# Performance work log

Hardware: AMD Instinct MI355X
Metric: run time of the kernel (lower is better)

## Reference

```python
import jax, jax.numpy as jnp
import numpy as np

M, N, B, L = 512, 2048, 4, 20
H_DENSITY = 0.02  # Tanner graph sparsity: row weight ~N*p=40, col weight ~M*p=10


def setup_inputs() -> dict:
    key = jax.random.key(0)
    ks = jax.random.split(key, 10)
    H = jax.random.bernoulli(ks[0], H_DENSITY, (M, N)).astype(jnp.float32)
    llrs = jax.random.uniform(ks[1], (N,), jnp.float32)
    syndromes = jax.random.randint(ks[2], (B, M, 1), 0, 2, jnp.int32)
    errors = jax.random.randint(ks[3], (B, N), 0, 2, jnp.int32)
    weights_de = jax.random.uniform(ks[4], (L, M, N), jnp.float32)
    weights_llr = jax.random.uniform(ks[5], (L, N), jnp.float32)
    marg_weights_de = jax.random.uniform(ks[6], (L, M, N), jnp.float32)
    marg_weights_llr = jax.random.uniform(ks[7], (L, N), jnp.float32)
    rhos = jnp.ones((L,), jnp.float32)
    residual_weights = jnp.zeros((L,), jnp.float32)
    return dict(syndromes=syndromes, errors=errors, H=H, llrs=llrs,
                weights_de=weights_de, weights_llr=weights_llr,
                marg_weights_de=marg_weights_de, marg_weights_llr=marg_weights_llr,
                rhos=rhos, residual_weights=residual_weights)


def reference(syndromes, errors, H, llrs, weights_de, weights_llr,
              marg_weights_de, marg_weights_llr, rhos, residual_weights):
    batch = syndromes.shape[0]
    m, n = H.shape
    rhos_norm = jax.nn.softmax(rhos)                       # (L,)
    sign = 1.0 - 2.0 * syndromes.astype(H.dtype)           # (B,m,1): (-1)**syndrome
    err_f = errors.astype(H.dtype)                         # (B,n)
    eps = 1e-6

    def step(msgs_dn, xs):
        w_de, w_llr, mw_de, mw_llr, rho, rw = xs
        # error-node (variable) update: column-sum minus self, masked by H
        msgs_en = (H * (llrs * w_llr)
                   + jnp.sum(msgs_dn * w_de, axis=1, keepdims=True)) * H - msgs_dn
        # detector-node (check) update: tanh-product rule with self-exclusion
        d = jnp.tanh(msgs_en * 0.5)
        d = jnp.where(d == 0, jnp.asarray(1.0, d.dtype), d)
        d = jnp.clip(d, -1.0 + eps, 1.0 - eps)
        row_prod = jnp.prod(d, axis=2, keepdims=True)      # (B,m,1)
        msgs_new = 2.0 * jnp.arctanh(row_prod / d) * (sign * H) + rw * msgs_dn
        # marginal beliefs and weighted BCE loss
        beliefs = jnp.sum(msgs_new * mw_de, axis=1) + llrs * mw_llr   # (B,n)
        loss_b = jnp.sum(jax.nn.softplus(beliefs) - (1.0 - err_f) * beliefs, axis=1)
        return msgs_new, rho * loss_b

    init = jnp.zeros((batch, m, n), H.dtype)
    _, losses = jax.lax.scan(
        step, init,
        (weights_de, weights_llr, marg_weights_de, marg_weights_llr,
         rhos_norm, residual_weights))
    return jnp.sum(losses) / batch
```

## Files before the change

### kernel.cpp

```cpp
#include <hip/hip_runtime.h>

#define MM 512
#define NN 2048
#define BB 4
#define LL 20
#define MAXDEG 128
#define NT    1024
#define RR    16
#define NBLK  64
#define COLSB 128
#define SLOTS 2048
#define EPT   2
#define EPSV  1e-6f

#define WS_ROW_DEG   0
#define WS_ROW_PAD   2048
#define WS_ROW_OFFF  264192
#define WS_RPTR_RB   266240
#define WS_EDGE_CS   299072
#define WS_WDE_P     430144
#define WS_MWDE_P    3051584
#define WS_PP        5673024
#define WS_BAR       5935168

__device__ __forceinline__ void pre_barrier(int* ctr) {
    __syncthreads();
    if (threadIdx.x == 0) {
        __threadfence();
        __hip_atomic_fetch_add(ctr, 1, __ATOMIC_RELAXED, __HIP_MEMORY_SCOPE_AGENT);
        int it = 0;
        while (__hip_atomic_load(ctr, __ATOMIC_RELAXED, __HIP_MEMORY_SCOPE_AGENT) < NBLK) {
            __builtin_amdgcn_s_sleep(1);
            if (++it > (1 << 22)) break;
        }
        __threadfence();
    }
    __syncthreads();
}

__device__ __forceinline__ void grid_barrier(int* ctr) {
    __syncthreads();
    if (threadIdx.x == 0) {
        asm volatile("s_waitcnt vmcnt(0)" ::: "memory");
        __hip_atomic_fetch_add(ctr, 1, __ATOMIC_RELAXED, __HIP_MEMORY_SCOPE_AGENT);
        int it = 0;
        while (__hip_atomic_load(ctr, __ATOMIC_RELAXED, __HIP_MEMORY_SCOPE_AGENT) < RR) {
            __builtin_amdgcn_s_sleep(1);
            if (++it > (1 << 22)) break;
        }
        asm volatile("" ::: "memory");
    }
    __syncthreads();
}

__global__ __launch_bounds__(NT)
void nbp_all(const int* __restrict__ synd, const int* __restrict__ errs,
             const float* __restrict__ H, const float* __restrict__ llrs,
             const float* __restrict__ w_de, const float* __restrict__ w_llr,
             const float* __restrict__ mw_de, const float* __restrict__ mw_llr,
             const float* __restrict__ rhos, const float* __restrict__ resw,
             int* __restrict__ row_deg, int* __restrict__ row_pad,
             float* __restrict__ row_offf, int* __restrict__ rptr_rb,
             unsigned* __restrict__ edge_cs,
             float* __restrict__ wde_p, float* __restrict__ mwde_p,
             float* __restrict__ pp, int* __restrict__ bar,
             float* __restrict__ out) {
    __shared__ float d_sb[SLOTS];
    __shared__ int   tmp_s[MM];
    __shared__ float colsum_s[COLSB];
    __shared__ float bel_s[COLSB];
    __shared__ float ncs_s[COLSB];
    __shared__ float llrs_s[COLSB];
    __shared__ float ef_s[COLSB];
    __shared__ float rowprod_s[MM];
    __shared__ float rp_coef[MM];
    __shared__ int   rowptr_s[MM + 1];
    __shared__ float rho_n[LL];
    __shared__ float red[16];

    const int blk = blockIdx.x;
    const int b = blk & 3, r = blk >> 2;
    const int tid = threadIdx.x;
    const int lane = tid & 63, wave = tid >> 6;
    int* bar_b = bar + b * 64;
    int* pbar  = bar + BB * 64;

    if (blk == 0 && tid == 0)
        __hip_atomic_store(out, 0.0f, __ATOMIC_RELAXED, __HIP_MEMORY_SCOPE_AGENT);

    if (wave < 8) {
        int i = blk * 8 + wave;
        const float* hrow = H + (size_t)i * NN;
        int base = 0;
        for (int pass = 0; pass < 4; ++pass) {
            float v[8];
            #pragma unroll
            for (int c = 0; c < 8; ++c) v[c] = hrow[(pass * 8 + c) * 64 + lane];
            #pragma unroll
            for (int c = 0; c < 8; ++c) {
                bool pred = v[c] != 0.0f;
                unsigned long long mask = __ballot(pred);
                int before = __popcll(mask & ((1ull << lane) - 1ull));
                if (pred) {
                    int k = base + before;
                    if (k < MAXDEG) row_pad[i * MAXDEG + k] = (pass * 8 + c) * 64 + lane;
                }
                base += __popcll(mask);
            }
        }
        if (lane == 0) {
            row_deg[i] = base < MAXDEG ? base : MAXDEG;
            row_offf[i] = powf(1.0f - EPSV, (float)(NN - base));
        }
    }
    pre_barrier(&pbar[0]);

    if (blk < RR) {
        const int slice = blk;
        if (tid < MM) {
            int deg = row_deg[tid], cnt = 0;
            for (int k = 0; k < deg; ++k)
                cnt += ((row_pad[tid * MAXDEG + k] >> 7) == slice);
            tmp_s[tid] = cnt;
        }
        __syncthreads();
        for (int off = 1; off < MM; off <<= 1) {
            int v = (tid < MM && tid >= off) ? tmp_s[tid - off] : 0;
            __syncthreads();
            if (tid < MM) tmp_s[tid] += v;
            __syncthreads();
        }
        if (tid == 0) rptr_rb[slice * 513] = 0;
        if (tid < MM) rptr_rb[slice * 513 + tid + 1] = tmp_s[tid];
        __syncthreads();
        if (tid < MM) {
            int deg = row_deg[tid];
            int pos = (tid == 0) ? 0 : tmp_s[tid - 1];
            for (int k = 0; k < deg; ++k) {
                int c = row_pad[tid * MAXDEG + k];
                if ((c >> 7) == slice && pos < SLOTS) {
                    edge_cs[slice * SLOTS + pos] = ((unsigned)tid << 16) | (unsigned)c;
                    ++pos;
                }
            }
        }
    }
    pre_barrier(&pbar[1]);

    for (int pr = blk; pr < LL * RR; pr += NBLK) {
        int l = pr / RR, slc = pr - l * RR;
        int tot = rptr_rb[slc * 513 + MM];
        if (tot > SLOTS) tot = SLOTS;
        const float* wl  = w_de + (size_t)l * (MM * NN);
        const float* mwl = mw_de + (size_t)l * (MM * NN);
        for (int s = tid; s < SLOTS; s += NT) {
            size_t di = (size_t)pr * SLOTS + s;
            if (s < tot) {
                unsigned pk = edge_cs[slc * SLOTS + s];
                size_t eo = (size_t)(pk >> 16) * NN + (pk & 0xffffu);
                wde_p[di]  = wl[eo];
                mwde_p[di] = mwl[eo];
            } else {
                wde_p[di]  = 0.0f;
                mwde_p[di] = 0.0f;
            }
        }
    }
    pre_barrier(&pbar[2]);

    if (tid == 0) {
        float mx = -1e30f;
        for (int l = 0; l < LL; ++l) mx = fmaxf(mx, rhos[l]);
        float s = 0.0f;
        for (int l = 0; l < LL; ++l) { float e = __expf(rhos[l] - mx); rho_n[l] = e; s += e; }
        for (int l = 0; l < LL; ++l) rho_n[l] /= s;
    }
    if (tid < MM) {
        rowptr_s[tid] = rptr_rb[r * 513 + tid];
        rp_coef[tid] = row_offf[tid] * (1.0f - 2.0f * (float)synd[b * MM + tid]);
    }
    if (tid == MM) rowptr_s[MM] = rptr_rb[r * 513 + MM];
    if (tid < COLSB) {
        int j = r * COLSB + tid;
        float lj = llrs[j];
        llrs_s[tid] = lj;
        colsum_s[tid] = lj * w_llr[j];
        ef_s[tid] = 1.0f - (float)errs[b * NN + j];
        bel_s[tid] = 0.0f;
        ncs_s[tid] = 0.0f;
    }

    int cnt = rptr_rb[r * 513 + MM];
    if (cnt > SLOTS) cnt = SLOTS;
    const int s0 = EPT * tid;

    unsigned idx[EPT];
    float msg[EPT], d_r[EPT];
    #pragma unroll
    for (int k = 0; k < EPT; ++k) {
        int e = r * SLOTS + s0 + k;
        idx[k] = edge_cs[(s0 + k) < cnt ? e : r * SLOTS];
        msg[k] = 0.0f;
    }
    __syncthreads();

    float loss = 0.0f;

    for (int l = 0; l < LL; ++l) {
        const float rw = resw[l];
        const int par = l & 1;
        float* pp_b = pp + ((size_t)par * BB + b) * RR * MM;

        const float2 mq = *(const float2*)(mwde_p + ((size_t)(l * RR + r) * SLOTS) + s0);
        float2 wq = make_float2(0.f, 0.f);
        if (l + 1 < LL)
            wq = *(const float2*)(wde_p + ((size_t)((l + 1) * RR + r) * SLOTS) + s0);
        const float mv[2] = {mq.x, mq.y};
        const float wn[2] = {wq.x, wq.y};

        #pragma unroll
        for (int k = 0; k < EPT; ++k) {
            int jl = idx[k] & (COLSB - 1);
            float en = colsum_s[jl] - msg[k];
            float t = __expf(en);
            float d = 1.0f - 2.0f * __builtin_amdgcn_rcpf(t + 1.0f);
            if (d == 0.0f) d = 1.0f;
            d = fminf(fmaxf(d, -1.0f + EPSV), 1.0f - EPSV);
            d_r[k] = d;
        }
        *(float2*)&d_sb[s0] = make_float2(d_r[0], d_r[1]);
        __syncthreads();

        if (tid < MM) {
            int lo = rowptr_s[tid], hi = rowptr_s[tid + 1];
            if (hi > SLOTS) hi = SLOTS;
            float p = 1.0f;
            for (int s = lo; s < hi; ++s) p *= d_sb[s];
            __hip_atomic_store(&pp_b[r * MM + tid], p,
                               __ATOMIC_RELAXED, __HIP_MEMORY_SCOPE_AGENT);
        }
        grid_barrier(&bar_b[l]);

        {
            int row = tid >> 1, half = tid & 1;
            float p = 1.0f;
            #pragma unroll
            for (int q = 0; q < RR / 2; ++q) {
                int r2 = q * 2 + half;
                p *= __hip_atomic_load(&pp_b[r2 * MM + row],
                                       __ATOMIC_RELAXED, __HIP_MEMORY_SCOPE_AGENT);
            }
            p *= __shfl_xor(p, 1);
            if (half == 0) rowprod_s[row] = p * rp_coef[row];
        }
        __syncthreads();

        #pragma unroll
        for (int k = 0; k < EPT; ++k) {
            int il = idx[k] >> 16;
            int jl = idx[k] & (COLSB - 1);
            float rq = rowprod_s[il] * __builtin_amdgcn_rcpf(d_r[k]);
            float v = __logf(1.0f + rq) - __logf(1.0f - rq) + rw * msg[k];
            msg[k] = v;
            if (s0 + k < cnt) {
                atomicAdd(&bel_s[jl], v * mv[k]);
                if (l + 1 < LL) atomicAdd(&ncs_s[jl], v * wn[k]);
            }
        }
        __syncthreads();

        if (tid < COLSB) {
            int j = r * COLSB + tid;
            float bel = llrs_s[tid] * mw_llr[l * NN + j] + bel_s[tid];
            bel_s[tid] = 0.0f;
            float sp = fmaxf(bel, 0.0f) + log1pf(__expf(-fabsf(bel)));
            loss += rho_n[l] * (sp - ef_s[tid] * bel);
            if (l + 1 < LL) {
                colsum_s[tid] = llrs_s[tid] * w_llr[(l + 1) * NN + j] + ncs_s[tid];
                ncs_s[tid] = 0.0f;
            }
        }
        __syncthreads();
    }

    #pragma unroll
    for (int off = 32; off > 0; off >>= 1) loss += __shfl_down(loss, off);
    if (lane == 0) red[wave] = loss;
    __syncthreads();
    if (wave == 0) {
        float v = (lane < 16) ? red[lane] : 0.0f;
        #pragma unroll
        for (int off = 8; off > 0; off >>= 1) v += __shfl_down(v, off);
        if (lane == 0) atomicAdd(out, v * 0.25f);
    }
}

extern "C" void kernel_launch(void* const* d_in, const int* in_sizes, int n_in,
                              void* d_out, int out_size, void* d_ws, size_t ws_size,
                              hipStream_t stream) {
    const int*   synd  = (const int*)  d_in[0];
    const int*   errs  = (const int*)  d_in[1];
    const float* H     = (const float*)d_in[2];
    const float* llrs  = (const float*)d_in[3];
    const float* w_de  = (const float*)d_in[4];
    const float* w_llr = (const float*)d_in[5];
    const float* mw_de = (const float*)d_in[6];
    const float* mw_llr= (const float*)d_in[7];
    const float* rhos  = (const float*)d_in[8];
    const float* resw  = (const float*)d_in[9];

    char* ws = (char*)d_ws;
    int*      row_deg  = (int*)     (ws + WS_ROW_DEG);
    int*      row_pad  = (int*)     (ws + WS_ROW_PAD);
    float*    row_offf = (float*)   (ws + WS_ROW_OFFF);
    int*      rptr_rb  = (int*)     (ws + WS_RPTR_RB);
    unsigned* edge_cs  = (unsigned*)(ws + WS_EDGE_CS);
    float*    wde_p    = (float*)   (ws + WS_WDE_P);
    float*    mwde_p   = (float*)   (ws + WS_MWDE_P);
    float*    pp       = (float*)   (ws + WS_PP);
    int*      bar      = (int*)     (ws + WS_BAR);
    float*    out      = (float*)d_out;

    hipMemsetAsync(bar, 0, (BB * 64 + 64) * sizeof(int), stream);

    nbp_all<<<NBLK, NT, 0, stream>>>(synd, errs, H, llrs, w_de, w_llr, mw_de, mw_llr,
                                     rhos, resw, row_deg, row_pad, row_offf, rptr_rb,
                                     edge_cs, wde_p, mwde_p, pp, bar, out);
}
```

Measured before the change: 395.3 us.

## Replace counter grid barrier with per-block flags and wave-parallel partial-product gathering

Drops the shared-counter grid barrier in favour of per-block monotonic flags, one per row-block within a batch. Each block publishes its flag after writing its partial row products. Each wave then waits on one peer's flag and copies that peer's partials into a shared staging buffer, and the rows are reduced locally from there. The mw_llr and w_llr loads are also hoisted to the top of the iteration so their latency is hidden. This shortens the synchronisation critical path and spreads the remote loads across waves, at the cost of 32KB more shared memory and a memory ordering that relies on relaxed atomics plus a spin without sleep.

```diff
diff --git a/kernel.cpp b/kernel.cpp
--- a/kernel.cpp
+++ b/kernel.cpp
@@ -34,21 +34,6 @@
             if (++it > (1 << 22)) break;
         }
         __threadfence();
-    }
-    __syncthreads();
-}
-
-__device__ __forceinline__ void grid_barrier(int* ctr) {
-    __syncthreads();
-    if (threadIdx.x == 0) {
-        asm volatile("s_waitcnt vmcnt(0)" ::: "memory");
-        __hip_atomic_fetch_add(ctr, 1, __ATOMIC_RELAXED, __HIP_MEMORY_SCOPE_AGENT);
-        int it = 0;
-        while (__hip_atomic_load(ctr, __ATOMIC_RELAXED, __HIP_MEMORY_SCOPE_AGENT) < RR) {
-            __builtin_amdgcn_s_sleep(1);
-            if (++it > (1 << 22)) break;
-        }
-        asm volatile("" ::: "memory");
     }
     __syncthreads();
 }
@@ -66,6 +51,7 @@
              float* __restrict__ pp, int* __restrict__ bar,
              float* __restrict__ out) {
     __shared__ float d_sb[SLOTS];
+    __shared__ float stage[RR * MM];
     __shared__ int   tmp_s[MM];
     __shared__ float colsum_s[COLSB];
     __shared__ float bel_s[COLSB];
@@ -82,8 +68,8 @@
     const int b = blk & 3, r = blk >> 2;
     const int tid = threadIdx.x;
     const int lane = tid & 63, wave = tid >> 6;
-    int* bar_b = bar + b * 64;
-    int* pbar  = bar + BB * 64;
+    int* flg  = bar + b * RR * 16;
+    int* pbar = bar + BB * RR * 16;
 
     if (blk == 0 && tid == 0)
         __hip_atomic_store(out, 0.0f, __ATOMIC_RELAXED, __HIP_MEMORY_SCOPE_AGENT);
@@ -217,6 +203,12 @@
             wq = *(const float2*)(wde_p + ((size_t)((l + 1) * RR + r) * SLOTS) + s0);
         const float mv[2] = {mq.x, mq.y};
         const float wn[2] = {wq.x, wq.y};
+        float mwl_r = 0.0f, wl_r = 0.0f;
+        if (tid < COLSB) {
+            int j = r * COLSB + tid;
+            mwl_r = mw_llr[l * NN + j];
+            if (l + 1 < LL) wl_r = w_llr[(l + 1) * NN + j];
+        }
 
         #pragma unroll
         for (int k = 0; k < EPT; ++k) {
@@ -238,20 +230,34 @@
             for (int s = lo; s < hi; ++s) p *= d_sb[s];
             __hip_atomic_store(&pp_b[r * MM + tid], p,
                                __ATOMIC_RELAXED, __HIP_MEMORY_SCOPE_AGENT);
-        }
-        grid_barrier(&bar_b[l]);
-
-        {
-            int row = tid >> 1, half = tid & 1;
-            float p = 1.0f;
+            stage[r * MM + tid] = p;
+        }
+        __syncthreads();
+        if (tid == 0)
+            __hip_atomic_store(&flg[r * 16], l + 1,
+                               __ATOMIC_RELAXED, __HIP_MEMORY_SCOPE_AGENT);
+
+        if (wave != r) {
+            int it = 0;
+            while (__hip_atomic_load(&flg[wave * 16], __ATOMIC_RELAXED,
+                                     __HIP_MEMORY_SCOPE_AGENT) < l + 1) {
+                if (++it > (1 << 20)) break;
+            }
             #pragma unroll
-            for (int q = 0; q < RR / 2; ++q) {
-                int r2 = q * 2 + half;
-                p *= __hip_atomic_load(&pp_b[r2 * MM + row],
-                                       __ATOMIC_RELAXED, __HIP_MEMORY_SCOPE_AGENT);
-            }
-            p *= __shfl_xor(p, 1);
-            if (half == 0) rowprod_s[row] = p * rp_coef[row];
+            for (int q = 0; q < MM / 64; ++q) {
+                int row = q * 64 + lane;
+                stage[wave * MM + row] =
+                    __hip_atomic_load(&pp_b[wave * MM + row],
+                                      __ATOMIC_RELAXED, __HIP_MEMORY_SCOPE_AGENT);
+            }
+        }
+        __syncthreads();
+
+        if (tid < MM) {
+            float p = rp_coef[tid];
+            #pragma unroll
+            for (int w = 0; w < RR; ++w) p *= stage[w * MM + tid];
+            rowprod_s[tid] = p;
         }
         __syncthreads();
 
@@ -270,13 +276,12 @@
         __syncthreads();
 
         if (tid < COLSB) {
-            int j = r * COLSB + tid;
-            float bel = llrs_s[tid] * mw_llr[l * NN + j] + bel_s[tid];
+            float bel = llrs_s[tid] * mwl_r + bel_s[tid];
             bel_s[tid] = 0.0f;
             float sp = fmaxf(bel, 0.0f) + log1pf(__expf(-fabsf(bel)));
             loss += rho_n[l] * (sp - ef_s[tid] * bel);
             if (l + 1 < LL) {
-                colsum_s[tid] = llrs_s[tid] * w_llr[(l + 1) * NN + j] + ncs_s[tid];
+                colsum_s[tid] = llrs_s[tid] * wl_r + ncs_s[tid];
                 ncs_s[tid] = 0.0f;
             }
         }
@@ -321,7 +326,7 @@
     int*      bar      = (int*)     (ws + WS_BAR);
     float*    out      = (float*)d_out;
 
-    hipMemsetAsync(bar, 0, (BB * 64 + 64) * sizeof(int), stream);
+    hipMemsetAsync(bar, 0, (BB * RR * 16 + 64) * sizeof(int), stream);
 
     nbp_all<<<NBLK, NT, 0, stream>>>(synd, errs, H, llrs, w_de, w_llr, mw_de, mw_llr,
                                      rhos, resw, row_deg, row_pad, row_offf, rptr_rb,
```

Measured after the change: 401.9 us. Within noise of the previous version (+1.7%).
